# Optimization experiments

Measured on AMD Instinct MI355X. Metric: run time of the kernel, lower is better.

## Reference

```python
import jax, jax.numpy as jnp
import numpy as np

B, L, D, U = 4, 1024, 64, 32

def setup_inputs() -> dict:
    key = jax.random.key(0)
    ks = jax.random.split(key, 6)
    inputs = jax.random.normal(ks[0], (B, L, D), dtype=jnp.float32)
    Wt = jax.random.normal(ks[1], (D, U), dtype=jnp.float32) * 0.1
    Wx = jax.random.normal(ks[2], (D, U), dtype=jnp.float32) * 0.1
    Wa = jax.random.normal(ks[3], (U, 1), dtype=jnp.float32) * 0.1
    bh = jax.random.normal(ks[4], (U,), dtype=jnp.float32) * 0.1
    ba = jax.random.normal(ks[5], (1,), dtype=jnp.float32) * 0.1
    return {"inputs": inputs, "Wt": Wt, "Wx": Wx, "Wa": Wa,
            "bh": bh, "ba": ba, "attention_width": 0}

def reference(inputs, Wt, Wx, Wa, bh, ba, attention_width):
    # Additive (Bahdanau) self-attention emission.
    q = inputs @ Wt                              # (B, L, U)
    k = inputs @ Wx                              # (B, L, U)
    # broadcast add -> (B, L, L, U), the dominant intermediate
    h = jnp.tanh(q[:, :, None, :] + k[:, None, :, :] + bh)
    e = jnp.squeeze(h @ Wa, axis=-1) + ba        # (B, L, L); ba broadcasts
    # NOTE: attention_width mask is dead code in the original forward -> ignored.
    # manual max-subtracted softmax with +1e-8 denominator (as in source)
    m = jnp.max(e, axis=-1, keepdims=True)
    ex = jnp.exp(e - m)
    a = ex / (jnp.sum(ex, axis=-1, keepdims=True) + 1e-8)
    v = jnp.einsum('bij,bjd->bid', a, inputs)    # (B, L, D)
    return v
```

## Files before the change

### kernel.cpp

```cpp
#include <hip/hip_runtime.h>

#define BB 4
#define LL 1024
#define DD 64
#define UU 32
#define TI 8
#define NT 512

typedef float f32x2 __attribute__((ext_vector_type(2)));
#define FMA2(a, b, c) __builtin_elementwise_fma((a), (b), (c))
static __device__ __forceinline__ f32x2 splat2(float x) { return (f32x2){x, x}; }

__global__ __launch_bounds__(256) void precompute_kernel(
    const float* __restrict__ inp, const float* __restrict__ Wt,
    const float* __restrict__ Wx, const float* __restrict__ bh,
    float* __restrict__ Eq, float* __restrict__ Ekt)
{
    __shared__ float s_in[8][DD];
    __shared__ float s_wt[DD][UU];
    __shared__ float s_wx[DD][UU];
    __shared__ float s_ek[8][36];
    int t = threadIdx.x;
    int row0 = blockIdx.x * 8;
    if (t < 128)
        ((float4*)s_in)[t] = ((const float4*)(inp + (size_t)row0 * DD))[t];
#pragma unroll
    for (int p = 0; p < 2; ++p) {
        ((float4*)s_wt)[p * 256 + t] = ((const float4*)Wt)[p * 256 + t];
        ((float4*)s_wx)[p * 256 + t] = ((const float4*)Wx)[p * 256 + t];
    }
    __syncthreads();
    int r = t >> 5;
    int u = t & 31;
    size_t row = row0 + r;
    float q = 0.f, k = 0.f;
#pragma unroll
    for (int d = 0; d < DD; ++d) {
        float x = s_in[r][d];
        q = fmaf(x, s_wt[d][u], q);
        k = fmaf(x, s_wx[d][u], k);
    }
    Eq[row * UU + u] = __expf(2.f * (q + bh[u]));
    s_ek[r][u] = __expf(2.f * k);
    __syncthreads();
    if (t < 64) {
        int u4 = t >> 3, r2 = t & 7;
        float4 v = *(const float4*)(&s_ek[r2][u4 * 4]);
        size_t gr = row0 + r2;
        size_t bb_ = gr >> 10, l = gr & 1023;
        ((float4*)Ekt)[(bb_ * 8 + u4) * LL + l] = v;
    }
}

__global__ __launch_bounds__(NT, 4) void attn_kernel(
    const float* __restrict__ Eq, const float* __restrict__ Ekt,
    const float* __restrict__ inp, const float* __restrict__ Wa,
    float* __restrict__ out)
{
    __shared__ float s_a0[LL][4];
    __shared__ float s_a1[LL][4];
    __shared__ float4 s_v[8][TI][16];
    __shared__ float s_red[8][TI];

    int t  = threadIdx.x;
    int w  = t >> 6;
    int b  = blockIdx.x >> 7;
    int i0 = (blockIdx.x & 127) * TI;

    const float4* ektb = (const float4*)Ekt + (size_t)b * 8 * LL;
    const float*  eqb  = Eq + ((size_t)(b * LL + i0)) * UU;

    f32x2 ekp[8][4];
#pragma unroll
    for (int u4 = 0; u4 < 8; ++u4) {
        float4 e0 = ektb[u4 * LL + t];
        float4 e1 = ektb[u4 * LL + NT + t];
        ekp[u4][0] = (f32x2){e0.x, e1.x};
        ekp[u4][1] = (f32x2){e0.y, e1.y};
        ekp[u4][2] = (f32x2){e0.z, e1.z};
        ekp[u4][3] = (f32x2){e0.w, e1.w};
    }

    const f32x2 ones = (f32x2){1.f, 1.f};
    f32x2 acc2[TI];
#pragma unroll
    for (int i = 0; i < TI; ++i) {
        acc2[i] = (f32x2){0.f, 0.f};
        const float* eqq = eqb + i * UU;
#pragma unroll
        for (int u4 = 0; u4 < 8; ++u4) {
            const float* waq = Wa + u4 * 4;
            f32x2 p = FMA2(splat2(eqq[u4 * 4 + 0]), ekp[u4][0], ones);
            f32x2 q = FMA2(splat2(eqq[u4 * 4 + 1]), ekp[u4][1], ones);
            f32x2 r = FMA2(splat2(eqq[u4 * 4 + 2]), ekp[u4][2], ones);
            f32x2 s = FMA2(splat2(eqq[u4 * 4 + 3]), ekp[u4][3], ones);
            f32x2 n01 = FMA2(splat2(waq[0]), q, splat2(waq[1]) * p);
            f32x2 n23 = FMA2(splat2(waq[2]), s, splat2(waq[3]) * r);
            f32x2 pq  = p * q;
            f32x2 rs2 = r * s;
            f32x2 num = FMA2(n01, rs2, n23 * pq);
            f32x2 den = pq * rs2;
            f32x2 rcpd;
            rcpd.x = __builtin_amdgcn_rcpf(den.x);
            rcpd.y = __builtin_amdgcn_rcpf(den.y);
            acc2[i] = FMA2(num, rcpd, acc2[i]);
        }
    }

    float wsum[TI];
#pragma unroll
    for (int i = 0; i < TI; ++i) {
        float e0 = __expf(-2.f * acc2[i].x);
        float e1 = __expf(-2.f * acc2[i].y);
        acc2[i].x = e0;
        acc2[i].y = e1;
        float s = e0 + e1;
#pragma unroll
        for (int mm = 32; mm >= 1; mm >>= 1) s += __shfl_xor(s, mm, 64);
        wsum[i] = s;
    }
    if ((t & 63) == 0) {
#pragma unroll
        for (int i = 0; i < TI; ++i) s_red[w][i] = wsum[i];
    }

    {
        float4 lo, hi;
        lo.x = acc2[0].x; lo.y = acc2[1].x; lo.z = acc2[2].x; lo.w = acc2[3].x;
        hi.x = acc2[4].x; hi.y = acc2[5].x; hi.z = acc2[6].x; hi.w = acc2[7].x;
        *(float4*)(&s_a0[t][0]) = lo;
        *(float4*)(&s_a1[t][0]) = hi;
        lo.x = acc2[0].y; lo.y = acc2[1].y; lo.z = acc2[2].y; lo.w = acc2[3].y;
        hi.x = acc2[4].y; hi.y = acc2[5].y; hi.z = acc2[6].y; hi.w = acc2[7].y;
        *(float4*)(&s_a0[NT + t][0]) = lo;
        *(float4*)(&s_a1[NT + t][0]) = hi;
    }
    __syncthreads();

    int dq = t & 15;
    int g  = t >> 4;
    const float4* inp4 = (const float4*)(inp + (size_t)b * LL * DD);
    f32x2 vac[4][4];
#pragma unroll
    for (int c = 0; c < 4; ++c)
#pragma unroll
        for (int p_ = 0; p_ < 4; ++p_) vac[c][p_] = (f32x2){0.f, 0.f};

#pragma unroll 4
    for (int jj = 0; jj < 32; ++jj) {
        int j = jj * 32 + g;
        float4 x  = inp4[j * 16 + dq];
        float4 a0 = *(const float4*)(&s_a0[j][0]);
        float4 a1 = *(const float4*)(&s_a1[j][0]);
        f32x2 ap0 = (f32x2){a0.x, a0.y};
        f32x2 ap1 = (f32x2){a0.z, a0.w};
        f32x2 ap2 = (f32x2){a1.x, a1.y};
        f32x2 ap3 = (f32x2){a1.z, a1.w};
        f32x2 xs;
        xs = splat2(x.x);
        vac[0][0] = FMA2(ap0, xs, vac[0][0]); vac[0][1] = FMA2(ap1, xs, vac[0][1]);
        vac[0][2] = FMA2(ap2, xs, vac[0][2]); vac[0][3] = FMA2(ap3, xs, vac[0][3]);
        xs = splat2(x.y);
        vac[1][0] = FMA2(ap0, xs, vac[1][0]); vac[1][1] = FMA2(ap1, xs, vac[1][1]);
        vac[1][2] = FMA2(ap2, xs, vac[1][2]); vac[1][3] = FMA2(ap3, xs, vac[1][3]);
        xs = splat2(x.z);
        vac[2][0] = FMA2(ap0, xs, vac[2][0]); vac[2][1] = FMA2(ap1, xs, vac[2][1]);
        vac[2][2] = FMA2(ap2, xs, vac[2][2]); vac[2][3] = FMA2(ap3, xs, vac[2][3]);
        xs = splat2(x.w);
        vac[3][0] = FMA2(ap0, xs, vac[3][0]); vac[3][1] = FMA2(ap1, xs, vac[3][1]);
        vac[3][2] = FMA2(ap2, xs, vac[3][2]); vac[3][3] = FMA2(ap3, xs, vac[3][3]);
    }

    float4 v[TI];
#pragma unroll
    for (int i = 0; i < TI; ++i) {
        int p_ = i >> 1;
        if (i & 1)
            v[i] = (float4){vac[0][p_].y, vac[1][p_].y, vac[2][p_].y, vac[3][p_].y};
        else
            v[i] = (float4){vac[0][p_].x, vac[1][p_].x, vac[2][p_].x, vac[3][p_].x};
    }

#pragma unroll
    for (int i = 0; i < TI; ++i) {
        v[i].x += __shfl_xor(v[i].x, 16, 64); v[i].y += __shfl_xor(v[i].y, 16, 64);
        v[i].z += __shfl_xor(v[i].z, 16, 64); v[i].w += __shfl_xor(v[i].w, 16, 64);
        v[i].x += __shfl_xor(v[i].x, 32, 64); v[i].y += __shfl_xor(v[i].y, 32, 64);
        v[i].z += __shfl_xor(v[i].z, 32, 64); v[i].w += __shfl_xor(v[i].w, 32, 64);
    }
    if ((t & 63) < 16) {
#pragma unroll
        for (int i = 0; i < TI; ++i) s_v[w][i][dq] = v[i];
    }
    __syncthreads();

    int i = t >> 6;
    int d = t & 63;
    const float* svf = (const float*)s_v;
    float r = 0.f;
#pragma unroll
    for (int w2 = 0; w2 < 8; ++w2) r += svf[w2 * (TI * 64) + i * 64 + d];
    float ssum = 0.f;
#pragma unroll
    for (int w2 = 0; w2 < 8; ++w2) ssum += s_red[w2][i];
    out[((size_t)b * LL + (i0 + i)) * DD + d] = r * (1.0f / (ssum + 1e-8f));
}

extern "C" void kernel_launch(void* const* d_in, const int* in_sizes, int n_in,
                              void* d_out, int out_size, void* d_ws, size_t ws_size,
                              hipStream_t stream) {
    const float* inp = (const float*)d_in[0];
    const float* Wt  = (const float*)d_in[1];
    const float* Wx  = (const float*)d_in[2];
    const float* Wa  = (const float*)d_in[3];
    const float* bh  = (const float*)d_in[4];
    float* out = (float*)d_out;

    float* Eq  = (float*)d_ws;
    float* Ekt = Eq + (size_t)BB * LL * UU;

    precompute_kernel<<<BB * LL / 8, 256, 0, stream>>>(inp, Wt, Wx, bh, Eq, Ekt);
    attn_kernel<<<BB * LL / TI, NT, 0, stream>>>(Eq, Ekt, inp, Wa, out);
}
```

Before: 88.74 us.

## Prefetch value rows, split reciprocal pairs, and enlarge precompute blocks

The precompute kernel now handles 16 rows per 512-thread block, so the weight-loading cost is spread over more rows. In the attention kernel, the single reciprocal of the four-term product is replaced by two reciprocals of two-term products with two accumulating FMAs. This removes a few multiplies but adds a transcendental instruction per pair. The value-pass loop is fully unrolled and software-prefetches the input rows four iterations ahead, with the first loads issued before the barrier to hide global latency, at the cost of more registers.

```diff
diff --git a/kernel.cpp b/kernel.cpp
--- a/kernel.cpp
+++ b/kernel.cpp
@@ -6,29 +6,27 @@
 #define UU 32
 #define TI 8
 #define NT 512
+#define PR 16
 
 typedef float f32x2 __attribute__((ext_vector_type(2)));
 #define FMA2(a, b, c) __builtin_elementwise_fma((a), (b), (c))
 static __device__ __forceinline__ f32x2 splat2(float x) { return (f32x2){x, x}; }
 
-__global__ __launch_bounds__(256) void precompute_kernel(
+__global__ __launch_bounds__(512) void precompute_kernel(
     const float* __restrict__ inp, const float* __restrict__ Wt,
     const float* __restrict__ Wx, const float* __restrict__ bh,
     float* __restrict__ Eq, float* __restrict__ Ekt)
 {
-    __shared__ float s_in[8][DD];
+    __shared__ float s_in[PR][DD];
     __shared__ float s_wt[DD][UU];
     __shared__ float s_wx[DD][UU];
-    __shared__ float s_ek[8][36];
+    __shared__ float s_ek[PR][36];
     int t = threadIdx.x;
-    int row0 = blockIdx.x * 8;
-    if (t < 128)
+    int row0 = blockIdx.x * PR;
+    ((float4*)s_wt)[t] = ((const float4*)Wt)[t];
+    ((float4*)s_wx)[t] = ((const float4*)Wx)[t];
+    if (t < 256)
         ((float4*)s_in)[t] = ((const float4*)(inp + (size_t)row0 * DD))[t];
-#pragma unroll
-    for (int p = 0; p < 2; ++p) {
-        ((float4*)s_wt)[p * 256 + t] = ((const float4*)Wt)[p * 256 + t];
-        ((float4*)s_wx)[p * 256 + t] = ((const float4*)Wx)[p * 256 + t];
-    }
     __syncthreads();
     int r = t >> 5;
     int u = t & 31;
@@ -43,8 +41,8 @@
     Eq[row * UU + u] = __expf(2.f * (q + bh[u]));
     s_ek[r][u] = __expf(2.f * k);
     __syncthreads();
-    if (t < 64) {
-        int u4 = t >> 3, r2 = t & 7;
+    if (t < 128) {
+        int u4 = t >> 4, r2 = t & 15;
         float4 v = *(const float4*)(&s_ek[r2][u4 * 4]);
         size_t gr = row0 + r2;
         size_t bb_ = gr >> 10, l = gr & 1023;
@@ -98,12 +96,13 @@
             f32x2 n23 = FMA2(splat2(waq[2]), s, splat2(waq[3]) * r);
             f32x2 pq  = p * q;
             f32x2 rs2 = r * s;
-            f32x2 num = FMA2(n01, rs2, n23 * pq);
-            f32x2 den = pq * rs2;
-            f32x2 rcpd;
-            rcpd.x = __builtin_amdgcn_rcpf(den.x);
-            rcpd.y = __builtin_amdgcn_rcpf(den.y);
-            acc2[i] = FMA2(num, rcpd, acc2[i]);
+            f32x2 rq, rr;
+            rq.x = __builtin_amdgcn_rcpf(pq.x);
+            rq.y = __builtin_amdgcn_rcpf(pq.y);
+            rr.x = __builtin_amdgcn_rcpf(rs2.x);
+            rr.y = __builtin_amdgcn_rcpf(rs2.y);
+            acc2[i] = FMA2(n01, rq, acc2[i]);
+            acc2[i] = FMA2(n23, rr, acc2[i]);
         }
     }
 
@@ -123,6 +122,14 @@
 #pragma unroll
         for (int i = 0; i < TI; ++i) s_red[w][i] = wsum[i];
     }
+
+    int dq = t & 15;
+    int g  = t >> 4;
+    const float4* inp4 = (const float4*)(inp + (size_t)b * LL * DD);
+    float4 xpre[4];
+#pragma unroll
+    for (int pf = 0; pf < 4; ++pf)
+        xpre[pf] = inp4[((pf * 32 + g) * 16) + dq];
 
     {
         float4 lo, hi;
@@ -137,19 +144,18 @@
     }
     __syncthreads();
 
-    int dq = t & 15;
-    int g  = t >> 4;
-    const float4* inp4 = (const float4*)(inp + (size_t)b * LL * DD);
     f32x2 vac[4][4];
 #pragma unroll
     for (int c = 0; c < 4; ++c)
 #pragma unroll
         for (int p_ = 0; p_ < 4; ++p_) vac[c][p_] = (f32x2){0.f, 0.f};
 
-#pragma unroll 4
+#pragma unroll
     for (int jj = 0; jj < 32; ++jj) {
         int j = jj * 32 + g;
-        float4 x  = inp4[j * 16 + dq];
+        float4 x = xpre[jj & 3];
+        if (jj + 4 < 32)
+            xpre[jj & 3] = inp4[(((jj + 4) * 32 + g) * 16) + dq];
         float4 a0 = *(const float4*)(&s_a0[j][0]);
         float4 a1 = *(const float4*)(&s_a1[j][0]);
         f32x2 ap0 = (f32x2){a0.x, a0.y};
@@ -219,6 +225,6 @@
     float* Eq  = (float*)d_ws;
     float* Ekt = Eq + (size_t)BB * LL * UU;
 
-    precompute_kernel<<<BB * LL / 8, 256, 0, stream>>>(inp, Wt, Wx, bh, Eq, Ekt);
+    precompute_kernel<<<BB * LL / PR, 512, 0, stream>>>(inp, Wt, Wx, bh, Eq, Ekt);
     attn_kernel<<<BB * LL / TI, NT, 0, stream>>>(Eq, Ekt, inp, Wa, out);
 }
```

New measurement: 90.57 us. 1.02x slower.
